# Kernel optimization log

Hardware: AMD Instinct MI355X
Metric: run time of the kernel (lower is better)

Reference implementation:

```python
import jax, jax.numpy as jnp
import numpy as np
from jax.lax import associative_scan

D_H = 512

def _binary_operator(e_i, e_j):
    a_i, kv_i = e_i
    a_j, kv_j = e_j
    return (a_j * a_i, a_j * kv_i + kv_j)

def setup_inputs() -> dict:
    key = jax.random.key(0)
    x = jax.random.normal(key, (4, 8192, 3 * D_H), dtype=jnp.float32)
    return {"x": x}

def reference(x):
    d_h = x.shape[-1] // 3
    inp = jnp.tanh(x[:, :, :d_h])
    gates = jax.nn.sigmoid(x[:, :, d_h:])
    input_gate, output_gate = jnp.split(gates, 2, axis=-1)
    forget_gate = 1.0 - input_gate
    # diagonal linear recurrence h_t = f_t * h_{t-1} + i_t * x_t via associative scan
    _, hidden_state = associative_scan(_binary_operator, (forget_gate, inp * input_gate), axis=1)
    return jnp.tanh(hidden_state) * output_gate
```

## Files before the change

### kernel.cpp

```cpp
#include <hip/hip_runtime.h>


#define B_   4
#define T_   8192
#define DH_  512
#define ROW4_ 384
#define DG4_  128

__device__ __forceinline__ float sigmoid_f(float x) {
    return __fdividef(1.0f, 1.0f + __expf(-x));
}

__device__ __forceinline__ float tanh_f(float x) {
    return 1.0f - __fdividef(2.0f, __expf(2.0f * x) + 1.0f);
}

__device__ __forceinline__ void step_agg(float xv, float gv, float& A, float& K) {
    const float s  = sigmoid_f(gv);
    const float f  = 1.0f - s;
    const float iv = tanh_f(xv) * s;
    A = f * A;
    K = f * K + iv;
}

__global__ __launch_bounds__(128) void k_partials(
        const float4* __restrict__ x4,
        float4* __restrict__ aggA,
        float4* __restrict__ aggKV,
        int C, int Tc) {
    const int c  = blockIdx.x;
    const int b  = blockIdx.y;
    const int d4 = threadIdx.x;
    const float4* xb = x4 + (size_t)b * T_ * ROW4_;
    const int t0 = c * Tc;

    float4 A  = make_float4(1.0f, 1.0f, 1.0f, 1.0f);
    float4 KV = make_float4(0.0f, 0.0f, 0.0f, 0.0f);
#pragma unroll 4
    for (int i = 0; i < Tc; ++i) {
        const size_t r = (size_t)(t0 + i) * ROW4_ + d4;
        const float4 xi = xb[r];
        const float4 gi = xb[r + DG4_];
        step_agg(xi.x, gi.x, A.x, KV.x);
        step_agg(xi.y, gi.y, A.y, KV.y);
        step_agg(xi.z, gi.z, A.z, KV.z);
        step_agg(xi.w, gi.w, A.w, KV.w);
    }
    const size_t idx = ((size_t)b * C + c) * DG4_ + d4;
    aggA[idx]  = A;
    aggKV[idx] = KV;
}

__global__ __launch_bounds__(128) void k_apply(
        const float4* __restrict__ x4,
        const float4* __restrict__ aggA,
        const float4* __restrict__ aggKV,
        float4* __restrict__ out4,
        int C, int Tc) {
    const int c  = blockIdx.x;
    const int b  = blockIdx.y;
    const int d4 = threadIdx.x;

    float4 h = make_float4(0.0f, 0.0f, 0.0f, 0.0f);
#pragma unroll 4
    for (int cc = 0; cc < c; ++cc) {
        const size_t idx = ((size_t)b * C + cc) * DG4_ + d4;
        const float4 a  = aggA[idx];
        const float4 kv = aggKV[idx];
        h.x = a.x * h.x + kv.x;
        h.y = a.y * h.y + kv.y;
        h.z = a.z * h.z + kv.z;
        h.w = a.w * h.w + kv.w;
    }

    const float4* xb = x4 + (size_t)b * T_ * ROW4_;
    float4* ob = out4 + (size_t)b * T_ * DG4_;
    const int t0 = c * Tc;

#pragma unroll 4
    for (int i = 0; i < Tc; ++i) {
        const size_t r = (size_t)(t0 + i) * ROW4_ + d4;
        const float4 xi = xb[r];
        const float4 gi = xb[r + DG4_];
        const float4 go = xb[r + 2 * DG4_];
        float4 o;
        {
            const float s = sigmoid_f(gi.x), f = 1.0f - s;
            h.x = f * h.x + tanh_f(xi.x) * s;
            o.x = tanh_f(h.x) * sigmoid_f(go.x);
        }
        {
            const float s = sigmoid_f(gi.y), f = 1.0f - s;
            h.y = f * h.y + tanh_f(xi.y) * s;
            o.y = tanh_f(h.y) * sigmoid_f(go.y);
        }
        {
            const float s = sigmoid_f(gi.z), f = 1.0f - s;
            h.z = f * h.z + tanh_f(xi.z) * s;
            o.z = tanh_f(h.z) * sigmoid_f(go.z);
        }
        {
            const float s = sigmoid_f(gi.w), f = 1.0f - s;
            h.w = f * h.w + tanh_f(xi.w) * s;
            o.w = tanh_f(h.w) * sigmoid_f(go.w);
        }
        ob[(size_t)(t0 + i) * DG4_ + d4] = o;
    }
}

extern "C" void kernel_launch(void* const* d_in, const int* in_sizes, int n_in,
                              void* d_out, int out_size, void* d_ws, size_t ws_size,
                              hipStream_t stream) {
    const float4* x4 = (const float4*)d_in[0];
    float4* out4 = (float4*)d_out;

    int C = 256;
    while (C > 1 && (size_t)B_ * C * DH_ * 2 * sizeof(float) > ws_size) C >>= 1;
    const int Tc = T_ / C;

    float4* aggA  = (float4*)d_ws;
    float4* aggKV = aggA + (size_t)B_ * C * DG4_;

    dim3 grid(C, B_);
    dim3 block(128);
    hipLaunchKernelGGL(k_partials, grid, block, 0, stream, x4, aggA, aggKV, C, Tc);
    hipLaunchKernelGGL(k_apply,    grid, block, 0, stream, x4, aggA, aggKV, out4, C, Tc);
}
```

Baseline: 346.7 us.

## Add separate chunk-prefix scan kernel and double chunk count

Adds a small k_scan kernel that computes each chunk's starting hidden state once per batch row and stores it. Before, every apply block re-walked all earlier chunk aggregates, which is quadratic work. The chunk count is fixed at 512 so each chunk is shorter and the grid is larger, and output stores become nontemporal. The cost is an extra launch and a serial 512-step scan on only 4 blocks. The workspace-size guard is removed, so the code assumes enough workspace is available.

```diff
diff --git a/kernel.cpp b/kernel.cpp
--- a/kernel.cpp
+++ b/kernel.cpp
@@ -1,16 +1,19 @@
 #include <hip/hip_runtime.h>
 
 
-#define B_   4
-#define T_   8192
-#define DH_  512
+#define B_    4
+#define T_    8192
+#define DH_   512
 #define ROW4_ 384
 #define DG4_  128
+#define C_    512
+#define TC_   (T_ / C_)
+
+typedef float nat4 __attribute__((ext_vector_type(4)));
 
 __device__ __forceinline__ float sigmoid_f(float x) {
     return __fdividef(1.0f, 1.0f + __expf(-x));
 }
-
 __device__ __forceinline__ float tanh_f(float x) {
     return 1.0f - __fdividef(2.0f, __expf(2.0f * x) + 1.0f);
 }
@@ -18,26 +21,24 @@
 __device__ __forceinline__ void step_agg(float xv, float gv, float& A, float& K) {
     const float s  = sigmoid_f(gv);
     const float f  = 1.0f - s;
-    const float iv = tanh_f(xv) * s;
     A = f * A;
-    K = f * K + iv;
+    K = f * K + tanh_f(xv) * s;
 }
 
 __global__ __launch_bounds__(128) void k_partials(
         const float4* __restrict__ x4,
         float4* __restrict__ aggA,
-        float4* __restrict__ aggKV,
-        int C, int Tc) {
+        float4* __restrict__ aggKV) {
     const int c  = blockIdx.x;
     const int b  = blockIdx.y;
     const int d4 = threadIdx.x;
     const float4* xb = x4 + (size_t)b * T_ * ROW4_;
-    const int t0 = c * Tc;
+    const int t0 = c * TC_;
 
     float4 A  = make_float4(1.0f, 1.0f, 1.0f, 1.0f);
     float4 KV = make_float4(0.0f, 0.0f, 0.0f, 0.0f);
 #pragma unroll 4
-    for (int i = 0; i < Tc; ++i) {
+    for (int i = 0; i < TC_; ++i) {
         const size_t r = (size_t)(t0 + i) * ROW4_ + d4;
         const float4 xi = xb[r];
         const float4 gi = xb[r + DG4_];
@@ -46,25 +47,22 @@
         step_agg(xi.z, gi.z, A.z, KV.z);
         step_agg(xi.w, gi.w, A.w, KV.w);
     }
-    const size_t idx = ((size_t)b * C + c) * DG4_ + d4;
+    const size_t idx = ((size_t)b * C_ + c) * DG4_ + d4;
     aggA[idx]  = A;
     aggKV[idx] = KV;
 }
 
-__global__ __launch_bounds__(128) void k_apply(
-        const float4* __restrict__ x4,
+__global__ __launch_bounds__(128) void k_scan(
         const float4* __restrict__ aggA,
         const float4* __restrict__ aggKV,
-        float4* __restrict__ out4,
-        int C, int Tc) {
-    const int c  = blockIdx.x;
-    const int b  = blockIdx.y;
+        float4* __restrict__ pref) {
+    const int b  = blockIdx.x;
     const int d4 = threadIdx.x;
 
     float4 h = make_float4(0.0f, 0.0f, 0.0f, 0.0f);
-#pragma unroll 4
-    for (int cc = 0; cc < c; ++cc) {
-        const size_t idx = ((size_t)b * C + cc) * DG4_ + d4;
+    for (int c = 0; c < C_; ++c) {
+        const size_t idx = ((size_t)b * C_ + c) * DG4_ + d4;
+        pref[idx] = h;
         const float4 a  = aggA[idx];
         const float4 kv = aggKV[idx];
         h.x = a.x * h.x + kv.x;
@@ -72,13 +70,24 @@
         h.z = a.z * h.z + kv.z;
         h.w = a.w * h.w + kv.w;
     }
+}
+
+__global__ __launch_bounds__(128) void k_apply(
+        const float4* __restrict__ x4,
+        const float4* __restrict__ pref,
+        float4* __restrict__ out4) {
+    const int c  = blockIdx.x;
+    const int b  = blockIdx.y;
+    const int d4 = threadIdx.x;
+
+    float4 h = pref[((size_t)b * C_ + c) * DG4_ + d4];
 
     const float4* xb = x4 + (size_t)b * T_ * ROW4_;
     float4* ob = out4 + (size_t)b * T_ * DG4_;
-    const int t0 = c * Tc;
+    const int t0 = c * TC_;
 
 #pragma unroll 4
-    for (int i = 0; i < Tc; ++i) {
+    for (int i = 0; i < TC_; ++i) {
         const size_t r = (size_t)(t0 + i) * ROW4_ + d4;
         const float4 xi = xb[r];
         const float4 gi = xb[r + DG4_];
@@ -104,7 +113,8 @@
             h.w = f * h.w + tanh_f(xi.w) * s;
             o.w = tanh_f(h.w) * sigmoid_f(go.w);
         }
-        ob[(size_t)(t0 + i) * DG4_ + d4] = o;
+        nat4 ov = {o.x, o.y, o.z, o.w};
+        __builtin_nontemporal_store(ov, (nat4*)&ob[(size_t)(t0 + i) * DG4_ + d4]);
     }
 }
 
@@ -114,15 +124,11 @@
     const float4* x4 = (const float4*)d_in[0];
     float4* out4 = (float4*)d_out;
 
-    int C = 256;
-    while (C > 1 && (size_t)B_ * C * DH_ * 2 * sizeof(float) > ws_size) C >>= 1;
-    const int Tc = T_ / C;
+    float4* aggA  = (float4*)d_ws;
+    float4* aggKV = aggA  + (size_t)B_ * C_ * DG4_;
+    float4* pref  = aggKV + (size_t)B_ * C_ * DG4_;
 
-    float4* aggA  = (float4*)d_ws;
-    float4* aggKV = aggA + (size_t)B_ * C * DG4_;
-
-    dim3 grid(C, B_);
-    dim3 block(128);
-    hipLaunchKernelGGL(k_partials, grid, block, 0, stream, x4, aggA, aggKV, C, Tc);
-    hipLaunchKernelGGL(k_apply,    grid, block, 0, stream, x4, aggA, aggKV, out4, C, Tc);
+    hipLaunchKernelGGL(k_partials, dim3(C_, B_), dim3(128), 0, stream, x4, aggA, aggKV);
+    hipLaunchKernelGGL(k_scan,     dim3(B_),     dim3(128), 0, stream, aggA, aggKV, pref);
+    hipLaunchKernelGGL(k_apply,    dim3(C_, B_), dim3(128), 0, stream, x4, pref, out4);
 }
```

New measurement: 363.2 us. +4.8%, slower.
